# Optimization experiments

Measured on AMD Instinct MI355X. Metric: run time of the kernel, lower is better.

Reference implementation:

```python
import jax, jax.numpy as jnp
import numpy as np

jax.config.update("jax_enable_x64", True)

NUM_OF_LSB_TO_IGNORE = 5
COMPARISON_NUM_BITS_IGNORED = 5
SCALE = 65536.0  # activations live on an integer-share-like scale so bit shifts matter

BLOCK_SIZES = np.array([[0, 1]] * 32 + [[2, 2]] * 48 + [[4, 4]] * 48)
# active (non-identity) block sizes and the channel indices they own
ACTIVE = [(tuple(int(v) for v in bs), np.where(np.all(BLOCK_SIZES == bs, axis=1))[0])
          for bs in np.unique(BLOCK_SIZES, axis=0) if 0 not in bs]


def setup_inputs() -> dict:
    key = jax.random.key(0)
    activation = jax.random.normal(key, (16, 128, 114, 114), dtype=jnp.float32) * SCALE
    return {"activation": activation}


def _block_sign(x, bh, bw):
    # x: [N, c, H, W]. Pad bottom/right to block multiples, space-to-depth,
    # integer floor-mean per block, LSB truncation via int16 wrap, sign >= 0.
    N, c, H, W = x.shape
    ph, pw = (-H) % bh, (-W) % bw
    xp = jnp.pad(x, ((0, 0), (0, 0), (0, ph), (0, pw)))
    xr = xp.reshape(N, c, (H + ph) // bh, bh, (W + pw) // bw, bw)
    s = xr.sum(axis=(3, 5)).astype(jnp.int64)          # block sums
    mean = s // (bh * bw)                               # integer floor mean
    q = ((mean >> NUM_OF_LSB_TO_IGNORE).astype(jnp.int16)
         .astype(jnp.int64)) << COMPARISON_NUM_BITS_IGNORED
    sign = q >= 0                                       # DReLU
    # broadcast block sign back to pixels, then unpad
    sign = jnp.repeat(jnp.repeat(sign, bh, axis=2), bw, axis=3)
    return sign[:, :, :H, :W]


def reference(activation):
    out = activation
    for (bh, bw), ch in ACTIVE:  # small fixed set of block-size groups
        cur = activation[:, ch]
        sign = _block_sign(cur, bh, bw)
        out = out.at[:, ch].set(cur * sign.astype(activation.dtype))
    return out
```

## Files before the change

### kernel.cpp

```cpp
#include <hip/hip_runtime.h>


#define NN 16
#define CC 128
#define HH 114
#define WW 114
#define PLANE (HH * WW)

__global__ __launch_bounds__(256) void copy_kernel(const float4* __restrict__ in,
                                                   float4* __restrict__ out) {
    const int per_n    = 32 * PLANE / 4;
    const int stride_n = CC * PLANE / 4;
    int idx = blockIdx.x * blockDim.x + threadIdx.x;
    if (idx >= NN * per_n) return;
    int n = idx / per_n;
    int r = idx - n * per_n;
    int off = n * stride_n + r;
    out[off] = in[off];
}

__global__ __launch_bounds__(256) void relu2_kernel(const float* __restrict__ in,
                                                    float* __restrict__ out) {
    int tid = blockIdx.x * blockDim.x + threadIdx.x;
    if (tid >= 768 * 3249) return;
    int plane = tid / 3249;
    int b     = tid - plane * 3249;
    int bh    = b / 57;
    int bw    = b - bh * 57;
    int n  = plane / 48;
    int c  = plane - n * 48;
    int base = (n * CC + 32 + c) * PLANE;
    int h0 = 2 * bh, w0 = 2 * bw;
    const float* p0 = in + base + h0 * WW + w0;
    const float* p1 = p0 + WW;
    float2 a = *(const float2*)p0;
    float2 d = *(const float2*)p1;
    float s = a.x + a.y + d.x + d.y;
    float m = (s > -1.0f) ? 1.0f : 0.0f;
    *(float2*)(out + base + h0 * WW + w0)       = make_float2(a.x * m, a.y * m);
    *(float2*)(out + base + (h0 + 1) * WW + w0) = make_float2(d.x * m, d.y * m);
}

__global__ __launch_bounds__(256) void relu4_kernel(const float* __restrict__ in,
                                                    float* __restrict__ out) {
    int tid = blockIdx.x * blockDim.x + threadIdx.x;
    if (tid >= 768 * 841) return;
    int plane = tid / 841;
    int b     = tid - plane * 841;
    int bh    = b / 29;
    int bw    = b - bh * 29;
    int n  = plane / 48;
    int c  = plane - n * 48;
    int base = (n * CC + 80 + c) * PLANE;
    int h0 = 4 * bh, w0 = 4 * bw;
    int nh = (h0 + 4 <= HH) ? 4 : (HH - h0);
    int nw = (w0 + 4 <= WW) ? 4 : (WW - w0);
    float x[4][4];
#pragma unroll
    for (int r = 0; r < 4; ++r) {
        if (r < nh) {
            const float* rp = in + base + (h0 + r) * WW + w0;
            float2 lo = *(const float2*)rp;
            x[r][0] = lo.x; x[r][1] = lo.y;
            if (nw == 4) {
                float2 hi = *(const float2*)(rp + 2);
                x[r][2] = hi.x; x[r][3] = hi.y;
            } else {
                x[r][2] = 0.0f; x[r][3] = 0.0f;
            }
        } else {
            x[r][0] = x[r][1] = x[r][2] = x[r][3] = 0.0f;
        }
    }
    float s = 0.0f;
#pragma unroll
    for (int r = 0; r < 4; ++r)
#pragma unroll
        for (int j = 0; j < 4; ++j) s += x[r][j];
    float m = (s > -1.0f) ? 1.0f : 0.0f;
    for (int r = 0; r < nh; ++r) {
        float* op = out + base + (h0 + r) * WW + w0;
        *(float2*)op = make_float2(x[r][0] * m, x[r][1] * m);
        if (nw == 4) *(float2*)(op + 2) = make_float2(x[r][2] * m, x[r][3] * m);
    }
}

extern "C" void kernel_launch(void* const* d_in, const int* in_sizes, int n_in,
                              void* d_out, int out_size, void* d_ws, size_t ws_size,
                              hipStream_t stream) {
    const float* in = (const float*)d_in[0];
    float* out = (float*)d_out;

    copy_kernel<<<6498, 256, 0, stream>>>((const float4*)in, (float4*)out);
    relu2_kernel<<<9747, 256, 0, stream>>>(in, out);
    relu4_kernel<<<2523, 256, 0, stream>>>(in, out);
}
```

Measured before the change: 196.9 us.

## Fuse copy and block-ReLU kernels into one launch with wider vector accesses

Merges the identity copy, 2x2 block and 4x4 block kernels into one launch that branches on block index, removing two kernel launches and their tail gaps. The 2x2 path now handles two horizontally adjacent blocks per thread, using float4 loads and stores on the top row. The 4x4 path uses float4 accesses on even rows, where the address is 16-byte aligned. Branch divergence stays per-block, so the cost in exchange is slightly more complex index math.

```diff
diff --git a/kernel.cpp b/kernel.cpp
--- a/kernel.cpp
+++ b/kernel.cpp
@@ -1,87 +1,114 @@
 #include <hip/hip_runtime.h>
 
 
-#define NN 16
 #define CC 128
-#define HH 114
 #define WW 114
-#define PLANE (HH * WW)
+#define PLANE 12996
 
-__global__ __launch_bounds__(256) void copy_kernel(const float4* __restrict__ in,
-                                                   float4* __restrict__ out) {
-    const int per_n    = 32 * PLANE / 4;
-    const int stride_n = CC * PLANE / 4;
-    int idx = blockIdx.x * blockDim.x + threadIdx.x;
-    if (idx >= NN * per_n) return;
-    int n = idx / per_n;
-    int r = idx - n * per_n;
-    int off = n * stride_n + r;
-    out[off] = in[off];
-}
+#define NBLK_A 6498
+#define NBLK_B 4959
+#define NBLK_C 2523
 
-__global__ __launch_bounds__(256) void relu2_kernel(const float* __restrict__ in,
-                                                    float* __restrict__ out) {
-    int tid = blockIdx.x * blockDim.x + threadIdx.x;
-    if (tid >= 768 * 3249) return;
-    int plane = tid / 3249;
-    int b     = tid - plane * 3249;
-    int bh    = b / 57;
-    int bw    = b - bh * 57;
-    int n  = plane / 48;
-    int c  = plane - n * 48;
-    int base = (n * CC + 32 + c) * PLANE;
-    int h0 = 2 * bh, w0 = 2 * bw;
-    const float* p0 = in + base + h0 * WW + w0;
-    const float* p1 = p0 + WW;
-    float2 a = *(const float2*)p0;
-    float2 d = *(const float2*)p1;
-    float s = a.x + a.y + d.x + d.y;
-    float m = (s > -1.0f) ? 1.0f : 0.0f;
-    *(float2*)(out + base + h0 * WW + w0)       = make_float2(a.x * m, a.y * m);
-    *(float2*)(out + base + (h0 + 1) * WW + w0) = make_float2(d.x * m, d.y * m);
-}
+__global__ __launch_bounds__(256) void fused_sbrelu_kernel(const float* __restrict__ in,
+                                                           float* __restrict__ out) {
+    const int bid = blockIdx.x;
+    const int tid = threadIdx.x;
 
-__global__ __launch_bounds__(256) void relu4_kernel(const float* __restrict__ in,
-                                                    float* __restrict__ out) {
-    int tid = blockIdx.x * blockDim.x + threadIdx.x;
-    if (tid >= 768 * 841) return;
-    int plane = tid / 841;
-    int b     = tid - plane * 841;
-    int bh    = b / 29;
-    int bw    = b - bh * 29;
-    int n  = plane / 48;
-    int c  = plane - n * 48;
-    int base = (n * CC + 80 + c) * PLANE;
-    int h0 = 4 * bh, w0 = 4 * bw;
-    int nh = (h0 + 4 <= HH) ? 4 : (HH - h0);
-    int nw = (w0 + 4 <= WW) ? 4 : (WW - w0);
-    float x[4][4];
+    if (bid < NBLK_A) {
+        int idx = bid * 256 + tid;
+        int n = idx / 103968;
+        int r = idx - n * 103968;
+        int off = n * 415872 + r;
+        ((float4*)out)[off] = ((const float4*)in)[off];
+    } else if (bid < NBLK_A + NBLK_B) {
+        int u = (bid - NBLK_A) * 256 + tid;
+        int plane = u / 1653;
+        int rest  = u - plane * 1653;
+        int r = rest / 29;
+        int j = rest - r * 29;
+        int n = plane / 48;
+        int c = plane - n * 48 + 32;
+        int base = (n * CC + c) * PLANE;
+        int e0 = 228 * r + 4 * j;
+        const float* bi = in + base;
+        float*       bo = out + base;
+        if (j < 28) {
+            float4 a  = *(const float4*)(bi + e0);
+            float2 b0 = *(const float2*)(bi + e0 + WW);
+            float2 b1 = *(const float2*)(bi + e0 + WW + 2);
+            float s0 = a.x + a.y + b0.x + b0.y;
+            float s1 = a.z + a.w + b1.x + b1.y;
+            float m0 = (s0 > -1.0f) ? 1.0f : 0.0f;
+            float m1 = (s1 > -1.0f) ? 1.0f : 0.0f;
+            *(float4*)(bo + e0)          = make_float4(a.x*m0, a.y*m0, a.z*m1, a.w*m1);
+            *(float2*)(bo + e0 + WW)     = make_float2(b0.x*m0, b0.y*m0);
+            *(float2*)(bo + e0 + WW + 2) = make_float2(b1.x*m1, b1.y*m1);
+        } else {
+            float2 a = *(const float2*)(bi + e0);
+            float2 b = *(const float2*)(bi + e0 + WW);
+            float s = a.x + a.y + b.x + b.y;
+            float m = (s > -1.0f) ? 1.0f : 0.0f;
+            *(float2*)(bo + e0)      = make_float2(a.x*m, a.y*m);
+            *(float2*)(bo + e0 + WW) = make_float2(b.x*m, b.y*m);
+        }
+    } else {
+        int u = (bid - NBLK_A - NBLK_B) * 256 + tid;
+        int plane = u / 841;
+        int rest  = u - plane * 841;
+        int bh = rest / 29;
+        int bw = rest - bh * 29;
+        int n = plane / 48;
+        int c = plane - n * 48 + 80;
+        int base = (n * CC + c) * PLANE;
+        int h0 = 4 * bh, w0 = 4 * bw;
+        int nh = (bh == 28) ? 2 : 4;
+        int nw = (bw == 28) ? 2 : 4;
+        const float* bi = in + base;
+        float*       bo = out + base;
+        float x[4][4];
 #pragma unroll
-    for (int r = 0; r < 4; ++r) {
-        if (r < nh) {
-            const float* rp = in + base + (h0 + r) * WW + w0;
-            float2 lo = *(const float2*)rp;
-            x[r][0] = lo.x; x[r][1] = lo.y;
-            if (nw == 4) {
-                float2 hi = *(const float2*)(rp + 2);
-                x[r][2] = hi.x; x[r][3] = hi.y;
+        for (int r = 0; r < 4; ++r) {
+            if (r < nh) {
+                int er = (h0 + r) * WW + w0;
+                if (nw == 4) {
+                    if ((r & 1) == 0) {
+                        float4 v = *(const float4*)(bi + er);
+                        x[r][0] = v.x; x[r][1] = v.y; x[r][2] = v.z; x[r][3] = v.w;
+                    } else {
+                        float2 lo = *(const float2*)(bi + er);
+                        float2 hi = *(const float2*)(bi + er + 2);
+                        x[r][0] = lo.x; x[r][1] = lo.y; x[r][2] = hi.x; x[r][3] = hi.y;
+                    }
+                } else {
+                    float2 lo = *(const float2*)(bi + er);
+                    x[r][0] = lo.x; x[r][1] = lo.y; x[r][2] = 0.0f; x[r][3] = 0.0f;
+                }
             } else {
-                x[r][2] = 0.0f; x[r][3] = 0.0f;
+                x[r][0] = x[r][1] = x[r][2] = x[r][3] = 0.0f;
             }
-        } else {
-            x[r][0] = x[r][1] = x[r][2] = x[r][3] = 0.0f;
         }
-    }
-    float s = 0.0f;
+        float s = 0.0f;
 #pragma unroll
-    for (int r = 0; r < 4; ++r)
+        for (int r = 0; r < 4; ++r)
 #pragma unroll
-        for (int j = 0; j < 4; ++j) s += x[r][j];
-    float m = (s > -1.0f) ? 1.0f : 0.0f;
-    for (int r = 0; r < nh; ++r) {
-        float* op = out + base + (h0 + r) * WW + w0;
-        *(float2*)op = make_float2(x[r][0] * m, x[r][1] * m);
-        if (nw == 4) *(float2*)(op + 2) = make_float2(x[r][2] * m, x[r][3] * m);
+            for (int j = 0; j < 4; ++j) s += x[r][j];
+        float m = (s > -1.0f) ? 1.0f : 0.0f;
+#pragma unroll
+        for (int r = 0; r < 4; ++r) {
+            if (r < nh) {
+                int er = (h0 + r) * WW + w0;
+                if (nw == 4) {
+                    if ((r & 1) == 0) {
+                        *(float4*)(bo + er) = make_float4(x[r][0]*m, x[r][1]*m, x[r][2]*m, x[r][3]*m);
+                    } else {
+                        *(float2*)(bo + er)     = make_float2(x[r][0]*m, x[r][1]*m);
+                        *(float2*)(bo + er + 2) = make_float2(x[r][2]*m, x[r][3]*m);
+                    }
+                } else {
+                    *(float2*)(bo + er) = make_float2(x[r][0]*m, x[r][1]*m);
+                }
+            }
+        }
     }
 }
 
@@ -90,8 +117,5 @@
                               hipStream_t stream) {
     const float* in = (const float*)d_in[0];
     float* out = (float*)d_out;
-
-    copy_kernel<<<6498, 256, 0, stream>>>((const float4*)in, (float4*)out);
-    relu2_kernel<<<9747, 256, 0, stream>>>(in, out);
-    relu4_kernel<<<2523, 256, 0, stream>>>(in, out);
+    fused_sbrelu_kernel<<<NBLK_A + NBLK_B + NBLK_C, 256, 0, stream>>>(in, out);
 }
```

Result: faster. 192.2 us (-2.4%).
